# Kernel optimization log

Measured on AMD Instinct MI355X. Metric: run time of the kernel, lower is better.

The kernel has to match this reference:

```python
import jax, jax.numpy as jnp
import numpy as np

N, E, F_IN, H, C = 10000, 320000, 256, 256, 40


def setup_inputs() -> dict:
    key = jax.random.key(0)
    ks = jax.random.split(key, 12)
    inp = {
        "x": jax.random.normal(ks[0], (N, F_IN), dtype=jnp.float32),
        "edge_index": jax.random.randint(ks[1], (2, E), 0, N, dtype=jnp.int64),
    }
    dims = [(F_IN, H), (H, H), (H, H), (H, H), (H, C)]
    for i, (din, dout) in enumerate(dims, start=1):
        scale = 1.0 / np.sqrt(din)
        inp[f"W{i}"] = jax.random.normal(ks[1 + i], (din, dout), dtype=jnp.float32) * scale
        inp[f"b{i}"] = jnp.zeros((dout,), dtype=jnp.float32)
    return inp


def _gcn_norm(edge_index, num_nodes, dtype):
    # GCNConv: add self-loops, symmetric normalization D^-1/2 (A+I) D^-1/2
    loops = jnp.arange(num_nodes, dtype=edge_index.dtype)
    src = jnp.concatenate([edge_index[0], loops])
    dst = jnp.concatenate([edge_index[1], loops])
    deg = jax.ops.segment_sum(jnp.ones_like(dst, dtype=dtype), dst, num_segments=num_nodes)
    dinv = jnp.where(deg > 0, deg ** -0.5, 0.0).astype(dtype)
    norm = dinv[src] * dinv[dst]  # [E+N]
    return src, dst, norm


def _conv(h, src, dst, norm, W, b, num_nodes):
    # linear transform then gather-scale-scatter aggregation
    h = h @ W                           # [N, dout]
    msg = h[src] * norm[:, None]        # [E+N, dout]
    return jax.ops.segment_sum(msg, dst, num_segments=num_nodes) + b


def reference(x, edge_index, W1, b1, W2, b2, W3, b3, W4, b4, W5, b5):
    num_nodes = x.shape[0]
    src, dst, norm = _gcn_norm(edge_index, num_nodes, x.dtype)
    h = jax.nn.relu(_conv(x, src, dst, norm, W1, b1, num_nodes))
    h = jax.nn.relu(_conv(h, src, dst, norm, W2, b2, num_nodes))
    h = jax.nn.relu(_conv(h, src, dst, norm, W3, b3, num_nodes))
    h = jax.nn.relu(_conv(h, src, dst, norm, W4, b4, num_nodes))
    logits = _conv(h, src, dst, norm, W5, b5, num_nodes)
    return jax.nn.log_softmax(logits, axis=1), logits
```

## Files before the change

kernel.cpp:

```cpp
#include <hip/hip_runtime.h>
#include <hip/hip_bf16.h>

#define N_NODES 10000
#define N_EDGES 320000
#define HDIM    256
#define NCLS    40

typedef __attribute__((ext_vector_type(8))) short short8;
typedef __attribute__((ext_vector_type(4))) float floatx4;
typedef unsigned long long ull;
typedef unsigned short ushort;

__device__ __forceinline__ float bf2f(ushort u) {
    union { unsigned int i; float f; } v; v.i = ((unsigned int)u) << 16; return v.f;
}
__device__ __forceinline__ ushort f2bf(float f) {
    __hip_bfloat16 h = __float2bfloat16(f);
    return *reinterpret_cast<ushort*>(&h);
}


__global__ void detect_kernel(const void* x, const void* ei, int* flags) {
    const int lane = threadIdx.x & 63;
    const ushort* u = (const ushort*)x;
    int e = (u[2 * lane] >> 7) & 0xFF;
    ull badmask = __ballot(e < 100 || e > 140);
    const int* ii = (const int*)ei;
    ull oddnz = __ballot(ii[2 * lane + 1] != 0);
    if (lane == 0) {
        flags[0] = (__popcll(badmask) >= 8) ? 1 : 0;
        flags[1] = (oddnz == 0) ? 1 : 0;
    }
}


struct PrepArgs {
    const void* x;
    const void* ei;
    const void* wsrc[10];
    ushort* wdst[10];
    int woffs[11];
    ushort* xb;
    int* src32;
    int* dst32;
    int* cnt;
    ushort* tbuf;
    ushort* hbuf;
    const int* flags;
};

#define PREP_XB 2500
#define PREP_WB 1069
#define PREP_EB 1250
#define PREP_ZB 40
#define PREP_SB 1
#define PREP_TOTAL (PREP_XB + PREP_WB + PREP_EB + PREP_ZB + PREP_SB)
#define WTOT 273448

__global__ __launch_bounds__(256)
void prep_kernel(PrepArgs a) {
    const int b = blockIdx.x;
    const int f32 = a.flags[0];
    if (b < PREP_XB) {
        int i4 = b * 256 + threadIdx.x;
        if (f32) {
            float4 v = ((const float4*)a.x)[i4];
            ull p = (ull)f2bf(v.x) | ((ull)f2bf(v.y) << 16) |
                    ((ull)f2bf(v.z) << 32) | ((ull)f2bf(v.w) << 48);
            ((ull*)a.xb)[i4] = p;
        } else {
            ((ull*)a.xb)[i4] = ((const ull*)a.x)[i4];
        }
    } else if (b < PREP_XB + PREP_WB) {
        int i = (b - PREP_XB) * 256 + threadIdx.x;
        if (i < WTOT) {
            int t = 0;
#pragma unroll
            for (int k = 1; k < 10; ++k) t += (i >= a.woffs[k]);
            int local = i - a.woffs[t];
            ushort v;
            if (f32) v = f2bf(((const float*)a.wsrc[t])[local]);
            else     v = ((const ushort*)a.wsrc[t])[local];
            a.wdst[t][local] = v;
        }
    } else if (b < PREP_XB + PREP_WB + PREP_EB) {
        int e = (b - PREP_XB - PREP_WB) * 256 + threadIdx.x;
        const int* ii = (const int*)a.ei;
        int s, d;
        if (a.flags[1]) { s = ii[2 * e]; d = ii[2 * (N_EDGES + e)]; }
        else            { s = ii[e];     d = ii[N_EDGES + e]; }
        a.src32[e] = ((unsigned)s < N_NODES) ? s : 0;
        a.dst32[e] = ((unsigned)d < N_NODES) ? d : 0;
    } else if (b < PREP_XB + PREP_WB + PREP_EB + PREP_ZB) {
        int i = (b - PREP_XB - PREP_WB - PREP_EB) * 256 + threadIdx.x;
        if (i < N_NODES) a.cnt[i] = 0;
    } else {
        int t = threadIdx.x;
        if (t < 64)       ((ull*)(a.tbuf + (size_t)N_NODES * 256))[t] = 0;
        else if (t < 128) ((ull*)(a.hbuf + (size_t)N_NODES * 256))[t - 64] = 0;
    }
}


__global__ void count_kernel(const int* __restrict__ dst, int* __restrict__ cnt) {
    int e = blockIdx.x * 256 + threadIdx.x;
    if (e < N_EDGES) atomicAdd(&cnt[dst[e]], 1);
}

__global__ __launch_bounds__(1024)
void scan_dinv_kernel(const int* __restrict__ cnt, int* __restrict__ offs,
                      int* __restrict__ woff, float* __restrict__ dinv) {
    __shared__ int part[1024];
    const int t = threadIdx.x;
    const int CH = (N_NODES + 1023) / 1024;
    const int base = t * CH;
    int s = 0;
    for (int j = 0; j < CH; ++j) {
        int i = base + j;
        if (i < N_NODES) s += cnt[i];
    }
    part[t] = s;
    __syncthreads();
    for (int off = 1; off < 1024; off <<= 1) {
        int v = 0;
        if (t >= off) v = part[t - off];
        __syncthreads();
        part[t] += v;
        __syncthreads();
    }
    int run = (t == 0) ? 0 : part[t - 1];
    for (int j = 0; j < CH; ++j) {
        int i = base + j;
        if (i < N_NODES) {
            int c = cnt[i];
            offs[i] = run;
            woff[i] = run;
            dinv[i] = rsqrtf((float)c + 1.0f);
            run += c;
        }
    }
}

__global__ void fill_kernel(const int* __restrict__ src, const int* __restrict__ dst,
                            int* __restrict__ woff, int* __restrict__ csr) {
    int e = blockIdx.x * 256 + threadIdx.x;
    if (e < N_EDGES) {
        int d = dst[e];
        int p = atomicAdd(&woff[d], 1);
        csr[p] = src[e];
    }
}


__global__ __launch_bounds__(256)
void gemm256_kernel(const ushort* __restrict__ A, const ushort* __restrict__ W,
                    const float* __restrict__ dinv, ushort* __restrict__ T) {
    const int lane = threadIdx.x & 63;
    const int wave = threadIdx.x >> 6;
    const int m = lane & 15;
    const int quad = lane >> 4;
    const int c0 = blockIdx.x * 32;

    short8 bfrag[2][8];
#pragma unroll
    for (int t = 0; t < 2; ++t)
#pragma unroll
        for (int s = 0; s < 8; ++s)
#pragma unroll
            for (int j = 0; j < 8; ++j)
                bfrag[t][s][j] = (short)W[(size_t)(s * 32 + quad * 8 + j) * 256 + c0 + t * 16 + m];

    const int step = gridDim.y * 4;
    for (int rt = blockIdx.y * 4 + wave; rt < N_NODES / 16; rt += step) {
        const int r0 = rt * 16;
        floatx4 acc0 = {0.f, 0.f, 0.f, 0.f};
        floatx4 acc1 = {0.f, 0.f, 0.f, 0.f};
        const ushort* arow = A + (size_t)(r0 + m) * 256 + quad * 8;
#pragma unroll
        for (int s = 0; s < 8; ++s) {
            short8 af = *(const short8*)(arow + s * 32);
            acc0 = __builtin_amdgcn_mfma_f32_16x16x32_bf16(af, bfrag[0][s], acc0, 0, 0, 0);
            acc1 = __builtin_amdgcn_mfma_f32_16x16x32_bf16(af, bfrag[1][s], acc1, 0, 0, 0);
        }
#pragma unroll
        for (int r = 0; r < 4; ++r) {
            int row = r0 + quad * 4 + r;
            float di = dinv[row];
            T[(size_t)row * 256 + c0 + m]      = f2bf(acc0[r] * di);
            T[(size_t)row * 256 + c0 + 16 + m] = f2bf(acc1[r] * di);
        }
    }
}


__global__ __launch_bounds__(256)
void gemm40_kernel(const ushort* __restrict__ A, const ushort* __restrict__ W,
                   const float* __restrict__ dinv, float* __restrict__ T) {
    const int lane = threadIdx.x & 63;
    const int wave = threadIdx.x >> 6;
    const int m = lane & 15;
    const int quad = lane >> 4;
    const int col = blockIdx.x * 16 + m;
    const bool colok = col < NCLS;

    short8 bfrag[8];
#pragma unroll
    for (int s = 0; s < 8; ++s)
#pragma unroll
        for (int j = 0; j < 8; ++j)
            bfrag[s][j] = colok ? (short)W[(size_t)(s * 32 + quad * 8 + j) * NCLS + col] : (short)0;

    const int step = gridDim.y * 4;
    for (int rt = blockIdx.y * 4 + wave; rt < N_NODES / 16; rt += step) {
        const int r0 = rt * 16;
        floatx4 acc = {0.f, 0.f, 0.f, 0.f};
        const ushort* arow = A + (size_t)(r0 + m) * 256 + quad * 8;
#pragma unroll
        for (int s = 0; s < 8; ++s) {
            short8 af = *(const short8*)(arow + s * 32);
            acc = __builtin_amdgcn_mfma_f32_16x16x32_bf16(af, bfrag[s], acc, 0, 0, 0);
        }
        if (colok) {
#pragma unroll
            for (int r = 0; r < 4; ++r) {
                int row = r0 + quad * 4 + r;
                T[(size_t)row * NCLS + col] = acc[r] * dinv[row];
            }
        }
    }
}


__device__ __forceinline__ void accum16(float* acc, int4 r) {
    int d[4] = {r.x, r.y, r.z, r.w};
#pragma unroll
    for (int k = 0; k < 4; ++k) {
        union { int i; float f; } lo, hi;
        lo.i = d[k] << 16;
        hi.i = d[k] & 0xffff0000;
        acc[2 * k]     += lo.f;
        acc[2 * k + 1] += hi.f;
    }
}

__global__ __launch_bounds__(256)
void agg256_kernel(const ushort* __restrict__ T,
                   const int* __restrict__ csr, const int* __restrict__ offs,
                   const int* __restrict__ cnt, const float* __restrict__ dinv,
                   const ushort* __restrict__ bias,
                   ushort* __restrict__ H) {
    const int node = blockIdx.x * 4 + (threadIdx.x >> 6);
    const int lane = threadIdx.x & 63;
    const int half = lane >> 5;
    const int q = lane & 31;
    const int start = offs[node];
    const int count = cnt[node];
    const float di = dinv[node];

    float acc[8];
    {
        int sinit = half ? N_NODES : node;
        int4 r = *(const int4*)(T + (size_t)sinit * 256 + q * 8);
#pragma unroll
        for (int k = 0; k < 4; ++k) {
            union { int i; float f; } lo, hi;
            int d = (&r.x)[k];
            lo.i = d << 16; hi.i = d & 0xffff0000;
            acc[2 * k] = lo.f; acc[2 * k + 1] = hi.f;
        }
    }

    for (int bj = 0; bj < count; bj += 64) {
        int mrem = count - bj;
        int mm = mrem < 64 ? mrem : 64;
        int idxv = (lane < mm) ? csr[start + bj + lane] : N_NODES;
        int j2 = 0;
        for (; j2 + 8 <= mm; j2 += 8) {
            int s0 = __shfl(idxv, j2 + half);
            int s1 = __shfl(idxv, j2 + 2 + half);
            int s2 = __shfl(idxv, j2 + 4 + half);
            int s3 = __shfl(idxv, j2 + 6 + half);
            int4 r0 = *(const int4*)(T + (size_t)s0 * 256 + q * 8);
            int4 r1 = *(const int4*)(T + (size_t)s1 * 256 + q * 8);
            int4 r2 = *(const int4*)(T + (size_t)s2 * 256 + q * 8);
            int4 r3 = *(const int4*)(T + (size_t)s3 * 256 + q * 8);
            accum16(acc, r0); accum16(acc, r1); accum16(acc, r2); accum16(acc, r3);
        }
        for (; j2 < mm; j2 += 2) {
            int s = __shfl(idxv, j2 + half);
            int4 r = *(const int4*)(T + (size_t)s * 256 + q * 8);
            accum16(acc, r);
        }
    }

#pragma unroll
    for (int i = 0; i < 8; ++i) acc[i] += __shfl_xor(acc[i], 32);

    if (half == 0) {
        int4 bv = *(const int4*)(bias + q * 8);
        int out_d[4];
#pragma unroll
        for (int k = 0; k < 4; ++k) {
            union { int i; float f; } lo, hi;
            int d = (&bv.x)[k];
            lo.i = d << 16; hi.i = d & 0xffff0000;
            float v0 = fmaxf(acc[2 * k] * di + lo.f, 0.f);
            float v1 = fmaxf(acc[2 * k + 1] * di + hi.f, 0.f);
            out_d[k] = (int)f2bf(v0) | ((int)f2bf(v1) << 16);
        }
        *(int4*)(H + (size_t)node * 256 + q * 8) = *(int4*)out_d;
    }
}


__global__ __launch_bounds__(256)
void aggsoft_kernel(const float* __restrict__ T,
                    const int* __restrict__ csr, const int* __restrict__ offs,
                    const int* __restrict__ cnt, const float* __restrict__ dinv,
                    const ushort* __restrict__ bias,
                    void* __restrict__ out, const int* __restrict__ flags) {
    const int node = blockIdx.x * 4 + (threadIdx.x >> 6);
    const int lane = threadIdx.x & 63;
    const int start = offs[node];
    const int count = cnt[node];
    const float di = dinv[node];

    float acc = (lane < NCLS) ? T[(size_t)node * NCLS + lane] : 0.f;
    for (int bj = 0; bj < count; bj += 64) {
        int mrem = count - bj;
        int mm = mrem < 64 ? mrem : 64;
        int idxv = (lane < mm) ? csr[start + bj + lane] : 0;
        int jj = 0;
        for (; jj + 4 <= mm; jj += 4) {
            int s0 = __shfl(idxv, jj + 0);
            int s1 = __shfl(idxv, jj + 1);
            int s2 = __shfl(idxv, jj + 2);
            int s3 = __shfl(idxv, jj + 3);
            if (lane < NCLS) {
                float t0 = T[(size_t)s0 * NCLS + lane];
                float t1 = T[(size_t)s1 * NCLS + lane];
                float t2 = T[(size_t)s2 * NCLS + lane];
                float t3 = T[(size_t)s3 * NCLS + lane];
                acc += t0 + t1 + t2 + t3;
            }
        }
        for (; jj < mm; ++jj) {
            int s = __shfl(idxv, jj);
            if (lane < NCLS) acc += T[(size_t)s * NCLS + lane];
        }
    }

    float l = (lane < NCLS) ? (acc * di + bf2f(bias[lane])) : -INFINITY;
    float mx = l;
#pragma unroll
    for (int o = 32; o > 0; o >>= 1) mx = fmaxf(mx, __shfl_xor(mx, o));
    float e = (lane < NCLS) ? __expf(l - mx) : 0.f;
    float sum = e;
#pragma unroll
    for (int o = 32; o > 0; o >>= 1) sum += __shfl_xor(sum, o);
    float ls = l - mx - __logf(sum);
    if (lane < NCLS) {
        size_t i0 = (size_t)node * NCLS + lane;
        size_t i1 = (size_t)N_NODES * NCLS + i0;
        if (flags[0]) {
            ((float*)out)[i0] = ls;
            ((float*)out)[i1] = l;
        } else {
            ((ushort*)out)[i0] = f2bf(ls);
            ((ushort*)out)[i1] = f2bf(l);
        }
    }
}


static inline size_t alup(size_t x) { return (x + 255) & ~(size_t)255; }

extern "C" void kernel_launch(void* const* d_in, const int* in_sizes, int n_in,
                              void* d_out, int out_size, void* d_ws, size_t ws_size,
                              hipStream_t stream) {
    char* w = (char*)d_ws;
    int* flags   = (int*)w;           w += alup(16);
    float* dinv  = (float*)w;         w += alup(N_NODES * 4);
    int* cnt     = (int*)w;           w += alup(N_NODES * 4);
    int* offs    = (int*)w;           w += alup(N_NODES * 4);
    int* woff    = (int*)w;           w += alup(N_NODES * 4);
    int* src32   = (int*)w;           w += alup(N_EDGES * 4);
    int* dst32   = (int*)w;           w += alup(N_EDGES * 4);
    int* csr     = (int*)w;           w += alup(N_EDGES * 4);
    ushort* xb   = (ushort*)w;        w += alup((size_t)N_NODES * HDIM * 2);
    ushort* wb[5]; ushort* bb[5];
    for (int l = 0; l < 5; ++l) {
        int wn = (l < 4) ? HDIM * HDIM : HDIM * NCLS;
        int bn = (l < 4) ? HDIM : NCLS;
        wb[l] = (ushort*)w; w += alup((size_t)wn * 2);
        bb[l] = (ushort*)w; w += alup((size_t)bn * 2);
    }
    ushort* tbuf = (ushort*)w;        w += alup((size_t)(N_NODES + 16) * HDIM * 2);
    ushort* hbuf = (ushort*)w;        w += alup((size_t)(N_NODES + 16) * HDIM * 2);
    float* t5    = (float*)w;         w += alup((size_t)N_NODES * NCLS * 4);

    detect_kernel<<<1, 64, 0, stream>>>(d_in[0], d_in[1], flags);

    PrepArgs pa;
    pa.x = d_in[0];
    pa.ei = d_in[1];
    int sizes[10] = { HDIM * HDIM, HDIM, HDIM * HDIM, HDIM, HDIM * HDIM, HDIM,
                      HDIM * HDIM, HDIM, HDIM * NCLS, NCLS };
    int run = 0;
    for (int t = 0; t < 10; ++t) {
        pa.wsrc[t] = d_in[2 + t];
        pa.wdst[t] = (t & 1) ? bb[t >> 1] : wb[t >> 1];
        pa.woffs[t] = run;
        run += sizes[t];
    }
    pa.woffs[10] = run;
    pa.xb = xb; pa.src32 = src32; pa.dst32 = dst32; pa.cnt = cnt;
    pa.tbuf = tbuf; pa.hbuf = hbuf; pa.flags = flags;

    prep_kernel<<<PREP_TOTAL, 256, 0, stream>>>(pa);

    const int eblk = (N_EDGES + 255) / 256;
    count_kernel<<<eblk, 256, 0, stream>>>(dst32, cnt);
    scan_dinv_kernel<<<1, 1024, 0, stream>>>(cnt, offs, woff, dinv);
    fill_kernel<<<eblk, 256, 0, stream>>>(src32, dst32, woff, csr);

    const int aggblk = N_NODES / 4;

    gemm256_kernel<<<dim3(8, 78), 256, 0, stream>>>(xb, wb[0], dinv, tbuf);
    agg256_kernel<<<aggblk, 256, 0, stream>>>(tbuf, csr, offs, cnt, dinv, bb[0], hbuf);
    for (int l = 1; l < 4; ++l) {
        gemm256_kernel<<<dim3(8, 78), 256, 0, stream>>>(hbuf, wb[l], dinv, tbuf);
        agg256_kernel<<<aggblk, 256, 0, stream>>>(tbuf, csr, offs, cnt, dinv, bb[l], hbuf);
    }
    gemm40_kernel<<<dim3(3, 80), 256, 0, stream>>>(hbuf, wb[4], dinv, t5);
    aggsoft_kernel<<<aggblk, 256, 0, stream>>>(t5, csr, offs, cnt, dinv, bb[4], d_out, flags);
}
```

Baseline: 276.5 us.

## Fuse detect/count into prep and fill with first GEMM to cut launches

Moves the format-detection step into every prep block, using shared-memory flags, and folds the degree counting (atomicAdd on cnt) into the edge-conversion blocks of prep. Zeroing cnt moves to a hipMemsetAsync. The CSR fill and the first-layer GEMM now run as one heterogeneous launch, since both only depend on the scan. The aim is to remove three kernel launches and their serialization gaps, and to overlap the atomic fill with MFMA work. The cost is redundant detection reads in every prep block, plus a memset still on the critical path.

```diff
diff --git a/kernel.cpp b/kernel.cpp
--- a/kernel.cpp
+++ b/kernel.cpp
@@ -5,6 +5,7 @@
 #define N_EDGES 320000
 #define HDIM    256
 #define NCLS    40
+#define WTOT    273448
 
 typedef __attribute__((ext_vector_type(8))) short short8;
 typedef __attribute__((ext_vector_type(4))) float floatx4;
@@ -19,18 +20,21 @@
     return *reinterpret_cast<ushort*>(&h);
 }
 
-
-__global__ void detect_kernel(const void* x, const void* ei, int* flags) {
-    const int lane = threadIdx.x & 63;
-    const ushort* u = (const ushort*)x;
-    int e = (u[2 * lane] >> 7) & 0xFF;
-    ull badmask = __ballot(e < 100 || e > 140);
-    const int* ii = (const int*)ei;
-    ull oddnz = __ballot(ii[2 * lane + 1] != 0);
-    if (lane == 0) {
-        flags[0] = (__popcll(badmask) >= 8) ? 1 : 0;
-        flags[1] = (oddnz == 0) ? 1 : 0;
-    }
+__device__ __forceinline__ void detect_flags(const void* x, const void* ei,
+                                             int* sflags) {
+    const int tid = threadIdx.x;
+    if (tid < 64) {
+        const ushort* u = (const ushort*)x;
+        int e = (u[2 * tid] >> 7) & 0xFF;
+        ull badmask = __ballot(e < 100 || e > 140);
+        const int* ii = (const int*)ei;
+        ull oddnz = __ballot(ii[2 * tid + 1] != 0);
+        if (tid == 0) {
+            sflags[0] = (__popcll(badmask) >= 8) ? 1 : 0;
+            sflags[1] = (oddnz == 0) ? 1 : 0;
+        }
+    }
+    __syncthreads();
 }
 
 
@@ -46,21 +50,21 @@
     int* cnt;
     ushort* tbuf;
     ushort* hbuf;
-    const int* flags;
+    int* flags;
 };
 
 #define PREP_XB 2500
 #define PREP_WB 1069
 #define PREP_EB 1250
-#define PREP_ZB 40
-#define PREP_SB 1
-#define PREP_TOTAL (PREP_XB + PREP_WB + PREP_EB + PREP_ZB + PREP_SB)
-#define WTOT 273448
+#define PREP_TOTAL (PREP_XB + PREP_WB + PREP_EB + 1)
 
 __global__ __launch_bounds__(256)
 void prep_kernel(PrepArgs a) {
+    __shared__ int sflags[2];
+    detect_flags(a.x, a.ei, sflags);
+    const int f32 = sflags[0];
     const int b = blockIdx.x;
-    const int f32 = a.flags[0];
+
     if (b < PREP_XB) {
         int i4 = b * 256 + threadIdx.x;
         if (f32) {
@@ -87,25 +91,21 @@
         int e = (b - PREP_XB - PREP_WB) * 256 + threadIdx.x;
         const int* ii = (const int*)a.ei;
         int s, d;
-        if (a.flags[1]) { s = ii[2 * e]; d = ii[2 * (N_EDGES + e)]; }
-        else            { s = ii[e];     d = ii[N_EDGES + e]; }
-        a.src32[e] = ((unsigned)s < N_NODES) ? s : 0;
-        a.dst32[e] = ((unsigned)d < N_NODES) ? d : 0;
-    } else if (b < PREP_XB + PREP_WB + PREP_EB + PREP_ZB) {
-        int i = (b - PREP_XB - PREP_WB - PREP_EB) * 256 + threadIdx.x;
-        if (i < N_NODES) a.cnt[i] = 0;
+        if (sflags[1]) { s = ii[2 * e]; d = ii[2 * (N_EDGES + e)]; }
+        else           { s = ii[e];     d = ii[N_EDGES + e]; }
+        s = ((unsigned)s < N_NODES) ? s : 0;
+        d = ((unsigned)d < N_NODES) ? d : 0;
+        a.src32[e] = s;
+        a.dst32[e] = d;
+        atomicAdd(&a.cnt[d], 1);
     } else {
         int t = threadIdx.x;
         if (t < 64)       ((ull*)(a.tbuf + (size_t)N_NODES * 256))[t] = 0;
         else if (t < 128) ((ull*)(a.hbuf + (size_t)N_NODES * 256))[t - 64] = 0;
-    }
-}
-
-
-__global__ void count_kernel(const int* __restrict__ dst, int* __restrict__ cnt) {
-    int e = blockIdx.x * 256 + threadIdx.x;
-    if (e < N_EDGES) atomicAdd(&cnt[dst[e]], 1);
-}
+        if (t == 0) { a.flags[0] = sflags[0]; a.flags[1] = sflags[1]; }
+    }
+}
+
 
 __global__ __launch_bounds__(1024)
 void scan_dinv_kernel(const int* __restrict__ cnt, int* __restrict__ offs,
@@ -141,13 +141,60 @@
     }
 }
 
-__global__ void fill_kernel(const int* __restrict__ src, const int* __restrict__ dst,
-                            int* __restrict__ woff, int* __restrict__ csr) {
-    int e = blockIdx.x * 256 + threadIdx.x;
-    if (e < N_EDGES) {
+
+#define FILL_BLKS 1250
+#define GEMM1_YT  78
+#define FG_TOTAL  (FILL_BLKS + 8 * GEMM1_YT)
+
+__global__ __launch_bounds__(256)
+void fillgemm_kernel(const int* __restrict__ src, const int* __restrict__ dst,
+                     int* __restrict__ woff, int* __restrict__ csr,
+                     const ushort* __restrict__ A, const ushort* __restrict__ W,
+                     const float* __restrict__ dinv, ushort* __restrict__ T) {
+    const int b = blockIdx.x;
+    if (b < FILL_BLKS) {
+        int e = b * 256 + threadIdx.x;
         int d = dst[e];
         int p = atomicAdd(&woff[d], 1);
         csr[p] = src[e];
+        return;
+    }
+    const int g = b - FILL_BLKS;
+    const int lane = threadIdx.x & 63;
+    const int wave = threadIdx.x >> 6;
+    const int m = lane & 15;
+    const int quad = lane >> 4;
+    const int c0 = (g & 7) * 32;
+    const int by = g >> 3;
+
+    short8 bfrag[2][8];
+#pragma unroll
+    for (int t = 0; t < 2; ++t)
+#pragma unroll
+        for (int s = 0; s < 8; ++s)
+#pragma unroll
+            for (int j = 0; j < 8; ++j)
+                bfrag[t][s][j] = (short)W[(size_t)(s * 32 + quad * 8 + j) * 256 + c0 + t * 16 + m];
+
+    const int step = GEMM1_YT * 4;
+    for (int rt = by * 4 + wave; rt < N_NODES / 16; rt += step) {
+        const int r0 = rt * 16;
+        floatx4 acc0 = {0.f, 0.f, 0.f, 0.f};
+        floatx4 acc1 = {0.f, 0.f, 0.f, 0.f};
+        const ushort* arow = A + (size_t)(r0 + m) * 256 + quad * 8;
+#pragma unroll
+        for (int s = 0; s < 8; ++s) {
+            short8 af = *(const short8*)(arow + s * 32);
+            acc0 = __builtin_amdgcn_mfma_f32_16x16x32_bf16(af, bfrag[0][s], acc0, 0, 0, 0);
+            acc1 = __builtin_amdgcn_mfma_f32_16x16x32_bf16(af, bfrag[1][s], acc1, 0, 0, 0);
+        }
+#pragma unroll
+        for (int r = 0; r < 4; ++r) {
+            int row = r0 + quad * 4 + r;
+            float di = dinv[row];
+            T[(size_t)row * 256 + c0 + m]      = f2bf(acc0[r] * di);
+            T[(size_t)row * 256 + c0 + 16 + m] = f2bf(acc1[r] * di);
+        }
     }
 }
 
@@ -399,7 +446,7 @@
     ushort* hbuf = (ushort*)w;        w += alup((size_t)(N_NODES + 16) * HDIM * 2);
     float* t5    = (float*)w;         w += alup((size_t)N_NODES * NCLS * 4);
 
-    detect_kernel<<<1, 64, 0, stream>>>(d_in[0], d_in[1], flags);
+    hipMemsetAsync(cnt, 0, N_NODES * 4, stream);
 
     PrepArgs pa;
     pa.x = d_in[0];
@@ -418,15 +465,12 @@
     pa.tbuf = tbuf; pa.hbuf = hbuf; pa.flags = flags;
 
     prep_kernel<<<PREP_TOTAL, 256, 0, stream>>>(pa);
-
-    const int eblk = (N_EDGES + 255) / 256;
-    count_kernel<<<eblk, 256, 0, stream>>>(dst32, cnt);
     scan_dinv_kernel<<<1, 1024, 0, stream>>>(cnt, offs, woff, dinv);
-    fill_kernel<<<eblk, 256, 0, stream>>>(src32, dst32, woff, csr);
+    fillgemm_kernel<<<FG_TOTAL, 256, 0, stream>>>(src32, dst32, woff, csr,
+                                                  xb, wb[0], dinv, tbuf);
 
     const int aggblk = N_NODES / 4;
 
-    gemm256_kernel<<<dim3(8, 78), 256, 0, stream>>>(xb, wb[0], dinv, tbuf);
     agg256_kernel<<<aggblk, 256, 0, stream>>>(tbuf, csr, offs, cnt, dinv, bb[0], hbuf);
     for (int l = 1; l < 4; ++l) {
         gemm256_kernel<<<dim3(8, 78), 256, 0, stream>>>(hbuf, wb[l], dinv, tbuf);
```

Result: faster. 269.1 us (-2.7%).
